# Kernel optimization log

Measured on AMD Instinct MI355X. Metric: run time of the kernel, lower is better.

The kernel has to match this reference:

```python
import jax, jax.numpy as jnp
import numpy as np

ORDER = 256     # N (HiPPO order)
A_DIAG = -0.5   # LagT: A = -(tril(ones) + a*I), a = -0.5
B_COEF = 1.0    # B = b * ones, b = 1


def toeplitz_mult(a, x):
    """Lower-triangular Toeplitz matvec = causal truncated convolution along last axis.
    a: (..., N) first column of the Toeplitz operator; x: (..., N)."""
    N = a.shape[-1]
    F = 2 * N
    af = jnp.fft.rfft(a, n=F, axis=-1)
    xf = jnp.fft.rfft(x, n=F, axis=-1)
    return jnp.fft.irfft(af * xf, n=F, axis=-1)[..., :N]


def forward_mult(u, delta):
    # (I + delta*A) u with A = -(tril(ones) + a*I):  u - delta*(cumsum(u) + a*u)
    return u - delta[..., None] * (jnp.cumsum(u, axis=-1) + A_DIAG * u)


def inverse_mult(u, delta):
    # (I - delta*A)^{-1} u. I - delta*A = c*I + delta*StrictLowerOnes, c = 1 + delta*(1+a).
    # Its inverse is lower-tri Toeplitz with first column [1/c, -(r/c), -(r/c)(1-r), ...], r = delta/c.
    N = u.shape[-1]
    d = delta[..., None]
    c = 1.0 + d * (1.0 + A_DIAG)
    r = d / c
    tail = -(r / c) * (1.0 - r) ** jnp.arange(N - 1, dtype=u.dtype)  # (..., N-1)
    kernel = jnp.concatenate([1.0 / c, tail], axis=-1)               # (..., N)
    return toeplitz_mult(kernel, u)


def bilinear(dt, u, v, alpha=0.5):
    # (I - alpha*dt*A)^{-1} [ (I + (1-alpha)*dt*A) u + dt * B * v ]
    x = forward_mult(u, (1.0 - alpha) * dt)
    x = x + (dt * v)[..., None] * B_COEF
    return inverse_mult(x, alpha * dt)


def setup_inputs() -> dict:
    key = jax.random.key(0)
    k1, k2 = jax.random.split(key)
    L, B, M = 1024, 4, 64
    inputs = jax.random.normal(k1, (L, B, M), dtype=jnp.float32)
    dt = jax.random.uniform(k2, (L, B, M), dtype=jnp.float32)
    return {"inputs": inputs, "dt": dt}


def reference(inputs, dt):
    L, B, M = inputs.shape
    N = ORDER
    e = jnp.zeros((N,), inputs.dtype).at[0].set(1.0)
    I = jnp.broadcast_to(e, (L, B, M, N))
    As = bilinear(dt, I, jnp.zeros_like(dt))       # (L,B,M,N) first columns of transition Toeplitz ops
    Bs = bilinear(dt, jnp.zeros_like(I), inputs)   # (L,B,M,N) discretized input contributions

    def step(x, ab):
        a, b = ab
        x = toeplitz_mult(a, x) + b                # x_l = A_l x_{l-1} + B_l  (variable_unroll_toeplitz)
        return x, x

    _, out = jax.lax.scan(step, jnp.zeros((B, M, N), inputs.dtype), (As, Bs))
    return out  # (L, B, M, N)
```

## Files before the change

kernel.cpp:

```cpp
#include <hip/hip_runtime.h>


namespace {

constexpr int LLEN   = 1024;
constexpr int NCHAN  = 256;
constexpr int KCH    = 32;
constexpr int SKEW   = 96;
constexpr int RSLOT  = 128;
constexpr int NCHUNK = 43;
constexpr int GPAD   = 1152;

constexpr int G_OFF = 0;
constexpr int B_OFF = GPAD;
constexpr int R_OFF = 2 * GPAD;
constexpr int LDS_FLOATS = R_OFF + 4 * RSLOT * 64;
constexpr size_t LDS_BYTES = (size_t)LDS_FLOATS * 4;

using f32x4 = __attribute__((ext_vector_type(4))) float;

__device__ __forceinline__ float dpp_shr1(float v) {
    return __int_as_float(__builtin_amdgcn_update_dpp(
        0, __float_as_int(v), 0x138 , 0xF, 0xF, false));
}
__device__ __forceinline__ float rdlane(float v, int s) {
    return __int_as_float(__builtin_amdgcn_readlane(__float_as_int(v), s));
}
__device__ __forceinline__ void compiler_mem_fence() {
    asm volatile("" ::: "memory");
}
__device__ __forceinline__ void lds_barrier() {
    __builtin_amdgcn_sched_barrier(0);
    asm volatile("s_waitcnt lgkmcnt(0)" ::: "memory");
    __builtin_amdgcn_s_barrier();
    __builtin_amdgcn_sched_barrier(0);
}

template <bool W0, bool MASKED>
__device__ __forceinline__ void do_chunk(
    const int T0, const int bl, const int lane, const bool lane0,
    const float* __restrict__ g_arr, const float* __restrict__ b_arr,
    const float* __restrict__ lf_ring, float* __restrict__ my_ring,
    float& g_cur, float& prev_own, float& prev_left)
{
    if (!MASKED) {
        f32x4 gb[8];
        const f32x4* gsrc = reinterpret_cast<const f32x4*>(g_arr + bl);
        #pragma unroll
        for (int q = 0; q < 8; ++q) gb[q] = gsrc[q];
        float hvv;
        if (W0) hvv = b_arr[T0 + (lane & 31)];
        else    hvv = lf_ring[(((bl + (lane & 31)) & (RSLOT - 1)) << 6) + 63];
        float hbs[KCH];
        #pragma unroll
        for (int s = 0; s < KCH; ++s) hbs[s] = rdlane(hvv, s);

        const int m0 = bl - lane;
        #pragma unroll
        for (int s = 0; s < KCH; ++s) {
            const float gj = dpp_shr1(g_cur);
            g_cur = lane0 ? gb[s >> 2][s & 3] : gj;
            const float u = dpp_shr1(prev_own);
            float cl, ct;
            if (W0) { cl = u;
                      ct = (lane0 ? hbs[s] : 0.0f) - prev_left; }
            else    { cl = u + (lane0 ? hbs[s] : 0.0f);
                      ct = 0.0f - prev_left; }
            const float x = fmaf(g_cur, cl, fmaf(g_cur, prev_own, ct));
            my_ring[(((m0 + s) & (RSLOT - 1)) << 6) + lane] = x;
            prev_left = cl;
            prev_own  = x;
        }
    } else {
        const int m0 = bl - lane;
        #pragma unroll
        for (int s = 0; s < KCH; ++s) {
            const int li = min(max(m0 + s, 0), LLEN - 1);
            const float gg = g_arr[li];
            float hb;
            if (W0) hb = b_arr[T0 + s];
            else    hb = lf_ring[(((bl + s) & (RSLOT - 1)) << 6) + 63];
            float cl = dpp_shr1(prev_own);
            float ct;
            if (W0) { ct = (lane0 ? hb : 0.0f) - prev_left; }
            else    { cl += lane0 ? hb : 0.0f;
                      ct = 0.0f - prev_left; }
            const float x = fmaf(gg, cl, fmaf(gg, prev_own, ct));
            my_ring[(((m0 + s) & (RSLOT - 1)) << 6) + lane] = x;
            const bool act = (unsigned)(m0 + s) < (unsigned)LLEN;
            prev_left = act ? cl : prev_left;
            prev_own  = act ? x  : prev_own;
        }
    }
}

__global__ __launch_bounds__(256, 1)
void toeplitz_scan(const float* __restrict__ vin,
                   const float* __restrict__ dtin,
                   float* __restrict__ out)
{
    extern __shared__ float lds[];
    float* g_arr = lds + G_OFF;
    float* b_arr = lds + B_OFF;
    float* ring  = lds + R_OFF;

    const int ch  = blockIdx.x;
    const int tid = threadIdx.x;

    #pragma unroll
    for (int k = 0; k < LLEN / 256; ++k) {
        const int l = tid + 256 * k;
        const float d = dtin[l * NCHAN + ch];
        const float u = vin[l * NCHAN + ch];
        const float ic = 1.0f / (1.0f + 0.25f * d);
        g_arr[l] = (1.0f - 0.25f * d) * ic;
        b_arr[l] = d * u * ic;
    }
    if (tid < GPAD - LLEN) {
        g_arr[LLEN + tid] = 1.0f;
        b_arr[LLEN + tid] = 0.0f;
    }
    __syncthreads();

    const int wave = tid >> 6, lane = tid & 63;
    const bool w0    = (wave == 0);
    const bool lane0 = (lane == 0);
    const int wskew  = wave * SKEW;

    float* my_ring = ring + wave * (RSLOT * 64);
    const float* lf_ring = ring + (wave > 0 ? (wave - 1) : 0) * (RSLOT * 64);

    float g_cur = 0.0f, prev_own = 0.0f, prev_left = 0.0f;

    const int rq = lane >> 4;
    const int cq = (lane & 15) << 2;
    float* const out_col = out + (size_t)(ch * 256 + wave * 64 + cq);

    for (int c = 0; c < NCHUNK; ++c) {
        const int T0 = c * KCH;
        const int bl = T0 - wskew;

        if (bl >= 0 && bl <= 1056) {
            const bool fast = (bl >= 64) && (bl <= LLEN - KCH);
            if (bl == 64) g_cur = g_arr[63 - lane];
            if (w0) {
                if (fast)
                    do_chunk<true, false>(T0, bl, lane, lane0, g_arr, b_arr,
                                          lf_ring, my_ring, g_cur,
                                          prev_own, prev_left);
                else
                    do_chunk<true, true>(T0, bl, lane, lane0, g_arr, b_arr,
                                         lf_ring, my_ring, g_cur,
                                         prev_own, prev_left);
            } else {
                if (fast)
                    do_chunk<false, false>(T0, bl, lane, lane0, g_arr, b_arr,
                                           lf_ring, my_ring, g_cur,
                                           prev_own, prev_left);
                else
                    do_chunk<false, true>(T0, bl, lane, lane0, g_arr, b_arr,
                                          lf_ring, my_ring, g_cur,
                                          prev_own, prev_left);
            }
        }

        const int F = T0 - wskew - 64;
        if (F >= 0 && F <= LLEN - KCH) {
            compiler_mem_fence();
            const float* rb = my_ring + ((F & (RSLOT - 1)) << 6) + cq;
            float* ob = out_col + (size_t)(F + rq) * (NCHAN * 256);
            #pragma unroll
            for (int q = 0; q < 8; ++q) {
                const f32x4 v =
                    *reinterpret_cast<const f32x4*>(rb + ((4 * q + rq) << 6));
                __builtin_nontemporal_store(v, reinterpret_cast<f32x4*>(ob));
                ob += (size_t)4 * (NCHAN * 256);
            }
        }
        lds_barrier();
    }
}

}

extern "C" void kernel_launch(void* const* d_in, const int* in_sizes, int n_in,
                              void* d_out, int out_size, void* d_ws, size_t ws_size,
                              hipStream_t stream) {
    (void)in_sizes; (void)n_in; (void)d_ws; (void)ws_size; (void)out_size;
    const float* vin  = (const float*)d_in[0];
    const float* dtin = (const float*)d_in[1];
    float* out = (float*)d_out;

    (void)hipFuncSetAttribute(reinterpret_cast<const void*>(toeplitz_scan),
                              hipFuncAttributeMaxDynamicSharedMemorySize,
                              (int)LDS_BYTES);

    toeplitz_scan<<<NCHAN, 256, LDS_BYTES, stream>>>(vin, dtin, out);
}
```

Measured before the change: 75.25 us.

## Read per-lane g and h values directly from LDS and issue output flush before compute

The fast chunk path now loads each lane's skewed g coefficients and boundary h values straight from LDS with ds_read2/ds_read_b128 inline asm. This replaces the DPP shift chain for g and the 32 readlane broadcasts for h. The output flush is moved ahead of the recurrence in each chunk and lags one chunk further, so global stores can overlap with the compute. NCHUNK grows by one to drain that extra lag. The price is more LDS read traffic, hand-written asm addressing that has to match the ring layout exactly, and one more loop iteration.

```diff
diff --git a/kernel.cpp b/kernel.cpp
--- a/kernel.cpp
+++ b/kernel.cpp
@@ -8,7 +8,7 @@
 constexpr int KCH    = 32;
 constexpr int SKEW   = 96;
 constexpr int RSLOT  = 128;
-constexpr int NCHUNK = 43;
+constexpr int NCHUNK = 44;
 constexpr int GPAD   = 1152;
 
 constexpr int G_OFF = 0;
@@ -18,16 +18,25 @@
 constexpr size_t LDS_BYTES = (size_t)LDS_FLOATS * 4;
 
 using f32x4 = __attribute__((ext_vector_type(4))) float;
+using f32x2 = __attribute__((ext_vector_type(2))) float;
 
 __device__ __forceinline__ float dpp_shr1(float v) {
     return __int_as_float(__builtin_amdgcn_update_dpp(
         0, __float_as_int(v), 0x138 , 0xF, 0xF, false));
 }
-__device__ __forceinline__ float rdlane(float v, int s) {
-    return __int_as_float(__builtin_amdgcn_readlane(__float_as_int(v), s));
-}
-__device__ __forceinline__ void compiler_mem_fence() {
-    asm volatile("" ::: "memory");
+__device__ __forceinline__ unsigned lds_a(const void* p) {
+    return (unsigned)(unsigned long long)p;
+}
+__device__ __forceinline__ void ds_rd128(f32x4& d, unsigned a, int imm) {
+    asm volatile("ds_read_b128 %0, %1 offset:%2" : "=v"(d) : "v"(a), "i"(imm));
+}
+__device__ __forceinline__ void ds_rd2(f32x2& d, unsigned a, int o0, int o1) {
+    asm volatile("ds_read2_b32 %0, %1 offset0:%2 offset1:%3"
+                 : "=v"(d) : "v"(a), "i"(o0), "i"(o1));
+}
+__device__ __forceinline__ void wait_lgkm0_fence() {
+    asm volatile("s_waitcnt lgkmcnt(0)" ::: "memory");
+    __builtin_amdgcn_sched_barrier(0);
 }
 __device__ __forceinline__ void lds_barrier() {
     __builtin_amdgcn_sched_barrier(0);
@@ -41,32 +50,41 @@
     const int T0, const int bl, const int lane, const bool lane0,
     const float* __restrict__ g_arr, const float* __restrict__ b_arr,
     const float* __restrict__ lf_ring, float* __restrict__ my_ring,
-    float& g_cur, float& prev_own, float& prev_left)
+    const unsigned g_base, const unsigned b_base, const unsigned lf_base,
+    float& prev_own, float& prev_left)
 {
     if (!MASKED) {
-        f32x4 gb[8];
-        const f32x4* gsrc = reinterpret_cast<const f32x4*>(g_arr + bl);
+        f32x2 g2[16], h2[16];
+        const unsigned ga = g_base + 4u * (unsigned)(bl - lane);
         #pragma unroll
-        for (int q = 0; q < 8; ++q) gb[q] = gsrc[q];
-        float hvv;
-        if (W0) hvv = b_arr[T0 + (lane & 31)];
-        else    hvv = lf_ring[(((bl + (lane & 31)) & (RSLOT - 1)) << 6) + 63];
-        float hbs[KCH];
-        #pragma unroll
-        for (int s = 0; s < KCH; ++s) hbs[s] = rdlane(hvv, s);
+        for (int q = 0; q < 16; ++q) ds_rd2(g2[q], ga, 2 * q, 2 * q + 1);
+        f32x4 hb4[8];
+        if (W0) {
+            const unsigned ba = b_base + 4u * (unsigned)T0;
+            #pragma unroll
+            for (int q = 0; q < 8; ++q) ds_rd128(hb4[q], ba, 16 * q);
+        } else {
+            const unsigned hbase = lf_base + ((unsigned)(bl & (RSLOT - 1)) << 8);
+            #pragma unroll
+            for (int q = 0; q < 8; ++q) {
+                const unsigned a = hbase + (unsigned)(q << 10);
+                ds_rd2(h2[2*q+0], a, 63, 127);
+                ds_rd2(h2[2*q+1], a, 191, 255);
+            }
+        }
+        wait_lgkm0_fence();
 
         const int m0 = bl - lane;
         #pragma unroll
         for (int s = 0; s < KCH; ++s) {
-            const float gj = dpp_shr1(g_cur);
-            g_cur = lane0 ? gb[s >> 2][s & 3] : gj;
-            const float u = dpp_shr1(prev_own);
-            float cl, ct;
-            if (W0) { cl = u;
-                      ct = (lane0 ? hbs[s] : 0.0f) - prev_left; }
-            else    { cl = u + (lane0 ? hbs[s] : 0.0f);
+            const float gg = g2[s >> 1][s & 1];
+            const float hb = W0 ? hb4[s >> 2][s & 3] : h2[s >> 1][s & 1];
+            float cl = dpp_shr1(prev_own);
+            float ct;
+            if (W0) { ct = (lane0 ? hb : 0.0f) - prev_left; }
+            else    { cl += lane0 ? hb : 0.0f;
                       ct = 0.0f - prev_left; }
-            const float x = fmaf(g_cur, cl, fmaf(g_cur, prev_own, ct));
+            const float x = fmaf(gg, cl, fmaf(gg, prev_own, ct));
             my_ring[(((m0 + s) & (RSLOT - 1)) << 6) + lane] = x;
             prev_left = cl;
             prev_own  = x;
@@ -129,8 +147,12 @@
 
     float* my_ring = ring + wave * (RSLOT * 64);
     const float* lf_ring = ring + (wave > 0 ? (wave - 1) : 0) * (RSLOT * 64);
-
-    float g_cur = 0.0f, prev_own = 0.0f, prev_left = 0.0f;
+    const unsigned g_base  = lds_a(g_arr);
+    const unsigned b_base  = lds_a(b_arr);
+    const unsigned my_base = lds_a(my_ring);
+    const unsigned lf_base = lds_a(lf_ring);
+
+    float prev_own = 0.0f, prev_left = 0.0f;
 
     const int rq = lane >> 4;
     const int cq = (lane & 15) << 2;
@@ -140,41 +162,43 @@
         const int T0 = c * KCH;
         const int bl = T0 - wskew;
 
+        const int F = bl - 96;
+        if (F >= 0 && F <= LLEN - KCH) {
+            f32x4 v[8];
+            const unsigned fb = my_base +
+                (unsigned)((((F & (RSLOT - 1)) + rq) << 8) + ((lane & 15) << 4));
+            #pragma unroll
+            for (int q = 0; q < 8; ++q) ds_rd128(v[q], fb, q * 1024);
+            wait_lgkm0_fence();
+            float* ob = out_col + (size_t)(F + rq) * (NCHAN * 256);
+            #pragma unroll
+            for (int q = 0; q < 8; ++q) {
+                __builtin_nontemporal_store(v[q], reinterpret_cast<f32x4*>(ob));
+                ob += (size_t)4 * (NCHAN * 256);
+            }
+            __builtin_amdgcn_sched_barrier(0);
+        }
+
         if (bl >= 0 && bl <= 1056) {
             const bool fast = (bl >= 64) && (bl <= LLEN - KCH);
-            if (bl == 64) g_cur = g_arr[63 - lane];
             if (w0) {
                 if (fast)
                     do_chunk<true, false>(T0, bl, lane, lane0, g_arr, b_arr,
-                                          lf_ring, my_ring, g_cur,
-                                          prev_own, prev_left);
+                                          lf_ring, my_ring, g_base, b_base,
+                                          lf_base, prev_own, prev_left);
                 else
                     do_chunk<true, true>(T0, bl, lane, lane0, g_arr, b_arr,
-                                         lf_ring, my_ring, g_cur,
-                                         prev_own, prev_left);
+                                         lf_ring, my_ring, g_base, b_base,
+                                         lf_base, prev_own, prev_left);
             } else {
                 if (fast)
                     do_chunk<false, false>(T0, bl, lane, lane0, g_arr, b_arr,
-                                           lf_ring, my_ring, g_cur,
-                                           prev_own, prev_left);
+                                           lf_ring, my_ring, g_base, b_base,
+                                           lf_base, prev_own, prev_left);
                 else
                     do_chunk<false, true>(T0, bl, lane, lane0, g_arr, b_arr,
-                                          lf_ring, my_ring, g_cur,
-                                          prev_own, prev_left);
-            }
-        }
-
-        const int F = T0 - wskew - 64;
-        if (F >= 0 && F <= LLEN - KCH) {
-            compiler_mem_fence();
-            const float* rb = my_ring + ((F & (RSLOT - 1)) << 6) + cq;
-            float* ob = out_col + (size_t)(F + rq) * (NCHAN * 256);
-            #pragma unroll
-            for (int q = 0; q < 8; ++q) {
-                const f32x4 v =
-                    *reinterpret_cast<const f32x4*>(rb + ((4 * q + rq) << 6));
-                __builtin_nontemporal_store(v, reinterpret_cast<f32x4*>(ob));
-                ob += (size_t)4 * (NCHAN * 256);
+                                          lf_ring, my_ring, g_base, b_base,
+                                          lf_base, prev_own, prev_left);
             }
         }
         lds_barrier();
```

After: 68.08 us. 9.5% less time.
